# Kernel tuning notes

Measured on AMD Instinct MI355X. Metric: run time of the kernel, lower is better.

Reference implementation:

```python
import jax, jax.numpy as jnp
import numpy as np

F_DIM = 128
EDGE_DIM = 41
N_CONV = 6
N_GRAPHS = 128
EPS = 1e-5


def _bn(h, g, b, m, v):
    # eval-mode BatchNorm1d with running stats
    return (h - m) * (g / jnp.sqrt(v + EPS)) + b


def setup_inputs() -> dict:
    key = jax.random.key(0)
    ks = jax.random.split(key, 40)
    N, E = 20000, 320000
    inp = {}
    inp['x'] = jax.random.normal(ks[0], (N, 98), dtype=jnp.float32)
    inp['edge_index'] = jax.random.randint(ks[1], (2, E), 0, N, dtype=jnp.int32)
    inp['edge_attr'] = jax.random.uniform(ks[2], (E, EDGE_DIM), dtype=jnp.float32)
    inp['batch'] = jnp.sort(jax.random.randint(ks[3], (N,), 0, N_GRAPHS, dtype=jnp.int32))
    s = 0.05
    inp['embed_W'] = jax.random.normal(ks[4], (98, F_DIM), dtype=jnp.float32) * s
    inp['embed_b'] = jnp.zeros((F_DIM,), jnp.float32)
    Z = 2 * F_DIM + EDGE_DIM  # 297
    inp['conv_Wf'] = jax.random.normal(ks[5], (N_CONV, Z, F_DIM), dtype=jnp.float32) * s
    inp['conv_bf'] = jnp.zeros((N_CONV, F_DIM), jnp.float32)
    inp['conv_Ws'] = jax.random.normal(ks[6], (N_CONV, Z, F_DIM), dtype=jnp.float32) * s
    inp['conv_bs'] = jnp.zeros((N_CONV, F_DIM), jnp.float32)
    # inner (CGConv) BN params + running stats
    inp['bn_in_g'] = jnp.ones((N_CONV, F_DIM), jnp.float32)
    inp['bn_in_b'] = jnp.zeros((N_CONV, F_DIM), jnp.float32)
    inp['bn_in_m'] = jax.random.normal(ks[7], (N_CONV, F_DIM), dtype=jnp.float32) * 0.1
    inp['bn_in_v'] = jax.random.uniform(ks[8], (N_CONV, F_DIM), dtype=jnp.float32) + 0.5
    # outer BN params + running stats
    inp['bn_out_g'] = jnp.ones((N_CONV, F_DIM), jnp.float32)
    inp['bn_out_b'] = jnp.zeros((N_CONV, F_DIM), jnp.float32)
    inp['bn_out_m'] = jax.random.normal(ks[9], (N_CONV, F_DIM), dtype=jnp.float32) * 0.1
    inp['bn_out_v'] = jax.random.uniform(ks[10], (N_CONV, F_DIM), dtype=jnp.float32) + 0.5
    inp['pool_W'] = jax.random.normal(ks[11], (2 * F_DIM, F_DIM), dtype=jnp.float32) * s
    inp['pool_b'] = jnp.zeros((F_DIM,), jnp.float32)
    inp['f1_W'] = jax.random.normal(ks[12], (F_DIM, 256), dtype=jnp.float32) * s
    inp['f1_b'] = jnp.zeros((256,), jnp.float32)
    inp['f2_W'] = jax.random.normal(ks[13], (256, 128), dtype=jnp.float32) * s
    inp['f2_b'] = jnp.zeros((128,), jnp.float32)
    inp['f3_W'] = jax.random.normal(ks[14], (128, 1), dtype=jnp.float32) * s
    inp['f3_b'] = jnp.zeros((1,), jnp.float32)
    inp['d1_W'] = jax.random.normal(ks[15], (F_DIM, 256), dtype=jnp.float32) * s
    inp['d1_b'] = jnp.zeros((256,), jnp.float32)
    inp['d2_W'] = jax.random.normal(ks[16], (256, 384), dtype=jnp.float32) * s
    inp['d2_b'] = jnp.zeros((384,), jnp.float32)
    return inp


def reference(x, edge_index, edge_attr, batch,
              embed_W, embed_b,
              conv_Wf, conv_bf, conv_Ws, conv_bs,
              bn_in_g, bn_in_b, bn_in_m, bn_in_v,
              bn_out_g, bn_out_b, bn_out_m, bn_out_v,
              pool_W, pool_b,
              f1_W, f1_b, f2_W, f2_b, f3_W, f3_b,
              d1_W, d1_b, d2_W, d2_b):
    N = x.shape[0]
    src, dst = edge_index[0], edge_index[1]  # PyG: messages flow src(j) -> dst(i)
    h = x @ embed_W + embed_b  # [N, F]
    for i in range(N_CONV):
        h_res = h
        # CGConv: z = [x_i, x_j, e_ij]; m = sigmoid(lin_f(z)) * softplus(lin_s(z))
        z = jnp.concatenate([h[dst], h[src], edge_attr], axis=-1)  # [E, 297]
        m = jax.nn.sigmoid(z @ conv_Wf[i] + conv_bf[i]) * jax.nn.softplus(z @ conv_Ws[i] + conv_bs[i])
        agg = jax.ops.segment_sum(m, dst, num_segments=N)  # scatter-add to target nodes
        agg = _bn(agg, bn_in_g[i], bn_in_b[i], bn_in_m[i], bn_in_v[i])  # CGConv internal BN
        h = agg + h  # CGConv residual
        h = _bn(h, bn_out_g[i], bn_out_b[i], bn_out_m[i], bn_out_v[i])  # outer BN
        if i > 0:
            h = h + h_res
        # dropout: identity in eval mode
    # global mean / max pool by graph id
    sums = jax.ops.segment_sum(h, batch, num_segments=N_GRAPHS)
    counts = jax.ops.segment_sum(jnp.ones((N,), h.dtype), batch, num_segments=N_GRAPHS)
    x_mean = sums / jnp.maximum(counts, 1.0)[:, None]
    x_max = jax.ops.segment_max(h, batch, num_segments=N_GRAPHS)
    x_max = jnp.where(jnp.isfinite(x_max), x_max, 0.0)
    x_pool = jnp.concatenate([x_mean, x_max], axis=-1)  # [B, 2F]
    emb = jax.nn.relu(x_pool @ pool_W + pool_b)  # [B, F]
    f = jax.nn.silu(emb @ f1_W + f1_b)
    f = jax.nn.silu(f @ f2_W + f2_b)
    formation = f @ f3_W + f3_b  # [B, 1]
    d = jax.nn.silu(emb @ d1_W + d1_b)
    dos = (d @ d2_W + d2_b).reshape(-1, 3, 128)  # [B, 3, 128]
    return formation, dos
```

## Files before the change

kernel.cpp:

```cpp
#include <hip/hip_runtime.h>
#include <hip/hip_bf16.h>
#include <math.h>

typedef __attribute__((ext_vector_type(8))) _Float16 half8;
typedef __attribute__((ext_vector_type(4))) _Float16 half4;
typedef __attribute__((ext_vector_type(4))) float f32x4;
typedef __attribute__((ext_vector_type(4))) unsigned int u32x4;

#define FDIM 128
#define EPSBN 1e-5f
#define HSCALE_INV 0.015625f
#define WSCALE 64.0f

__global__ void prep_wn(const float* __restrict__ Wf, const float* __restrict__ Ws,
                        _Float16* __restrict__ Wn) {
    int idx = blockIdx.x * 256 + threadIdx.x;
    const int total = 6 * 4 * 512 * 32;
    if (idx >= total) return;
    int kk = idx & 31;
    int col = (idx >> 5) & 511;
    int c4 = (idx >> 14) & 3;
    int i = idx >> 16;
    int which = col >> 8;
    int colc = col & 255;
    int p = (colc >> 4) & 1;
    int f = ((colc >> 5) << 4) | (colc & 15);
    int ksrc = c4 * 32 + (kk ^ ((colc & 3) << 3));
    int row = which * 128 + ksrc;
    size_t o = ((size_t)i * 297 + row) * 128 + f;
    float v = (p ? Ws[o] : Wf[o]) * WSCALE;
    Wn[idx] = (_Float16)v;
}

__global__ void prep_wb2(const float* __restrict__ Wf, const float* __restrict__ Ws,
                         _Float16* __restrict__ Wb2) {
    int idx = blockIdx.x * 256 + threadIdx.x;
    const int total = 6 * 16384;
    if (idx >= total) return;
    int j = idx & 7;
    int l15 = (idx >> 3) & 15;
    int lhi = (idx >> 7) & 3;
    int cb = (idx >> 9) & 15;
    int c2 = (idx >> 13) & 1;
    int i = idx >> 14;
    int k = c2 * 32 + lhi * 8 + j;
    int colc = cb * 16 + l15;
    int p = (colc >> 4) & 1;
    int f = ((colc >> 5) << 4) | (colc & 15);
    float v = 0.0f;
    if (k < 41) {
        size_t o = ((size_t)i * 297 + 256 + k) * 128 + f;
        v = p ? Ws[o] : Wf[o];
    }
    Wb2[idx] = (_Float16)v;
}

__global__ void prep_bn(const float* __restrict__ bing, const float* __restrict__ binb,
                        const float* __restrict__ binm, const float* __restrict__ binv,
                        const float* __restrict__ bog, const float* __restrict__ bob,
                        const float* __restrict__ bom, const float* __restrict__ bov,
                        float* __restrict__ ABC) {
    int idx = blockIdx.x * 128 + threadIdx.x;
    if (idx >= 6 * 128) return;
    int f = idx & 127;
    int i = idx >> 7;
    int o = i * 128 + f;
    float gin_ = bing[o] / sqrtf(binv[o] + EPSBN);
    float gout_ = bog[o] / sqrtf(bov[o] + EPSBN);
    float A = gin_ * gout_;
    float B = gout_ + ((i > 0) ? 1.0f : 0.0f);
    float C = (binb[o] - binm[o] * gin_ - bom[o]) * gout_ + bob[o];
    ABC[i * 384 + f] = A;
    ABC[i * 384 + 128 + f] = B;
    ABC[i * 384 + 256 + f] = C;
}

__global__ void hist_k(const int* __restrict__ dstI, int* __restrict__ cnt, int E) {
    int e = blockIdx.x * 256 + threadIdx.x;
    if (e < E) atomicAdd(&cnt[dstI[e]], 1);
}

__global__ void scan_k(const int* __restrict__ cnt, int* __restrict__ cursor, int N) {
    __shared__ int part[256];
    int t = threadIdx.x;
    int chunk = (N + 255) / 256;
    int lo = t * chunk, hi = lo + chunk; if (hi > N) hi = N;
    int s = 0;
    for (int i = lo; i < hi; ++i) s += cnt[i];
    part[t] = s;
    __syncthreads();
    for (int d = 1; d < 256; d <<= 1) {
        int v = (t >= d) ? part[t - d] : 0;
        __syncthreads();
        part[t] += v;
        __syncthreads();
    }
    int run = (t > 0) ? part[t - 1] : 0;
    for (int i = lo; i < hi; ++i) { cursor[i] = run; run += cnt[i]; }
}

__global__ void scatter_k(const int* __restrict__ srcI, const int* __restrict__ dstI,
                          int* __restrict__ cursor, unsigned* __restrict__ sdS,
                          int* __restrict__ perm, int E) {
    int e = blockIdx.x * 256 + threadIdx.x;
    if (e >= E) return;
    int d = dstI[e];
    int pos = atomicAdd(&cursor[d], 1);
    sdS[pos] = (unsigned)srcI[e] | ((unsigned)d << 16);
    perm[pos] = e;
}

__global__ void permute_ea(const float* __restrict__ ea, const int* __restrict__ perm,
                           _Float16* __restrict__ eaH, int E) {
    int pos = blockIdx.x * 4 + (threadIdx.x >> 6);
    int c = threadIdx.x & 63;
    if (pos >= E) return;
    int e = perm[pos];
    float v = (c < 41) ? ea[(size_t)e * 41 + c] : 0.0f;
    eaH[(size_t)pos * 64 + c] = (_Float16)v;
}

__global__ void embed_k(const float* __restrict__ x, const float* __restrict__ W,
                        const float* __restrict__ b, float* __restrict__ h, int N) {
    int n = blockIdx.x * 2 + (threadIdx.x >> 7);
    int f = threadIdx.x & 127;
    if (n >= N) return;
    float acc = b[f];
    const float* xr = x + (size_t)n * 98;
    #pragma unroll 7
    for (int k = 0; k < 98; ++k) acc = fmaf(xr[k], W[k * 128 + f], acc);
    h[(size_t)n * 128 + f] = acc;
}

__global__ __launch_bounds__(256, 2)
void node_gemm_f(float* __restrict__ h, float* __restrict__ agg,
                 const _Float16* __restrict__ WnL, const float* __restrict__ ABC,
                 float* __restrict__ Pd4, float* __restrict__ Ps4, int N, int doBN) {
    __shared__ __align__(16) _Float16 ht[32 * 128];
    __shared__ __align__(16) _Float16 wt[512 * 32];
    const int tid = threadIdx.x;
    const int nb = blockIdx.x * 32;

    {
        int e = tid >> 3, t = tid & 7;
        int node = nb + e; bool ok = (node < N); if (!ok) node = N - 1;
        const int c0 = t * 16;
        float* hrow = h + (size_t)node * 128 + c0;
        __align__(16) _Float16 tmp[16];
        if (doBN && ok) {
            float* arow = agg + (size_t)node * 128 + c0;
            #pragma unroll
            for (int u = 0; u < 16; u += 4) {
                f32x4 av = *(const f32x4*)(arow + u);
                f32x4 hv = *(const f32x4*)(hrow + u);
                f32x4 Av = *(const f32x4*)(ABC + c0 + u);
                f32x4 Bv = *(const f32x4*)(ABC + 128 + c0 + u);
                f32x4 Cv = *(const f32x4*)(ABC + 256 + c0 + u);
                f32x4 x;
                #pragma unroll
                for (int j = 0; j < 4; ++j)
                    x[j] = fmaf(av[j], Av[j], fmaf(hv[j], Bv[j], Cv[j]));
                *(f32x4*)(hrow + u) = x;
                *(f32x4*)(arow + u) = (f32x4){0.f, 0.f, 0.f, 0.f};
                #pragma unroll
                for (int j = 0; j < 4; ++j) tmp[u + j] = (_Float16)(x[j] * HSCALE_INV);
            }
        } else {
            #pragma unroll
            for (int u = 0; u < 16; u += 4) {
                f32x4 hv = *(const f32x4*)(hrow + u);
                #pragma unroll
                for (int j = 0; j < 4; ++j) tmp[u + j] = (_Float16)(hv[j] * HSCALE_INV);
            }
        }
        int swz = (e & 7) << 4;
        *(u32x4*)((char*)ht + e * 256 + (((2 * t) * 16) ^ swz)) = *(u32x4*)tmp;
        *(u32x4*)((char*)ht + e * 256 + (((2 * t + 1) * 16) ^ swz)) = *(u32x4*)(tmp + 8);
    }

    f32x4 acc[2][8];
    #pragma unroll
    for (int m = 0; m < 2; ++m)
        #pragma unroll
        for (int n = 0; n < 8; ++n) acc[m][n] = (f32x4){0.f, 0.f, 0.f, 0.f};

    const int wid = tid >> 6;
    const int lane = tid & 63;
    const int l15 = lane & 15;
    const int lhi = lane >> 4;
    const int swzA = (l15 & 7) << 4;

    for (int c4 = 0; c4 < 4; ++c4) {
        const u32x4* gw = (const u32x4*)(WnL + (size_t)c4 * 512 * 32);
        #pragma unroll
        for (int j = 0; j < 8; ++j) ((u32x4*)wt)[tid + 256 * j] = gw[tid + 256 * j];
        __syncthreads();

        half8 a[2];
        #pragma unroll
        for (int m = 0; m < 2; ++m) {
            int r = m * 16 + l15;
            a[m] = *(const half8*)((const char*)ht + r * 256 + ((c4 * 64 + lhi * 16) ^ swzA));
        }
        #pragma unroll
        for (int n = 0; n < 8; ++n) {
            int col = wid * 128 + n * 16 + l15;
            half8 b = *(const half8*)((const char*)wt + col * 64 + ((lhi * 16) ^ ((col & 3) << 4)));
            #pragma unroll
            for (int m = 0; m < 2; ++m)
                acc[m][n] = __builtin_amdgcn_mfma_f32_16x16x32_f16(a[m], b, acc[m][n], 0, 0, 0);
        }
        __syncthreads();
    }

    #pragma unroll
    for (int m = 0; m < 2; ++m) {
        #pragma unroll
        for (int n = 0; n < 8; ++n) {
            int col512 = wid * 128 + n * 16 + l15;
            float* base = (col512 < 256) ? Pd4 : Ps4;
            int c = col512 & 255;
            int g = ((c >> 6) << 4) | (c & 15);
            int q = (c >> 4) & 3;
            #pragma unroll
            for (int j = 0; j < 4; ++j) {
                int node = nb + m * 16 + lhi * 4 + j;
                if (node < N) base[(size_t)node * 256 + g * 4 + q] = acc[m][n][j];
            }
        }
    }
}

__global__ __launch_bounds__(256, 4)
void edge_v7(const _Float16* __restrict__ eaH,
             const unsigned* __restrict__ sdS,
             const _Float16* __restrict__ WbL,
             const float* __restrict__ Pd4, const float* __restrict__ Ps4,
             const float* __restrict__ biasF, const float* __restrict__ biasS,
             float* __restrict__ agg) {
    __shared__ __align__(16) _Float16 eacc[64 * 256];
    __shared__ int srcl[64], dstl[64];

    const int tid = threadIdx.x;
    const int eb = blockIdx.x * 64;

    if (tid < 64) {
        unsigned sd = sdS[eb + tid];
        srcl[tid] = (int)(sd & 0xFFFFu);
        dstl[tid] = (int)(sd >> 16);
    }

    const int wid = tid >> 6;
    const int lane = tid & 63;
    const int l15 = lane & 15;
    const int lhi = lane >> 4;

    f32x4 acc[4][4];
    #pragma unroll
    for (int m = 0; m < 4; ++m)
        #pragma unroll
        for (int n = 0; n < 4; ++n) acc[m][n] = (f32x4){0.f, 0.f, 0.f, 0.f};

    #pragma unroll
    for (int c2 = 0; c2 < 2; ++c2) {
        half8 a[4];
        #pragma unroll
        for (int m = 0; m < 4; ++m) {
            int r = m * 16 + l15;
            a[m] = *(const half8*)(eaH + (size_t)(eb + r) * 64 + c2 * 32 + lhi * 8);
        }
        #pragma unroll
        for (int n = 0; n < 4; ++n) {
            int cb = wid * 4 + n;
            const half8 b = *(const half8*)(WbL +
                            ((((size_t)c2 * 16 + cb) * 4 + lhi) * 16 + l15) * 8);
            #pragma unroll
            for (int m = 0; m < 4; ++m)
                acc[m][n] = __builtin_amdgcn_mfma_f32_16x16x32_f16(a[m], b, acc[m][n], 0, 0, 0);
        }
    }

    {
        const int g = (wid << 4) | l15;
        #pragma unroll
        for (int m = 0; m < 4; ++m) {
            #pragma unroll
            for (int j = 0; j < 4; ++j) {
                int r = m * 16 + lhi * 4 + j;
                half4 hv;
                hv[0] = (_Float16)acc[m][0][j];
                hv[1] = (_Float16)acc[m][1][j];
                hv[2] = (_Float16)acc[m][2][j];
                hv[3] = (_Float16)acc[m][3][j];
                *(half4*)(eacc + r * 256 + g * 4) = hv;
            }
        }
    }
    __syncthreads();

    const int f0 = ((lane >> 4) << 5) | l15;
    const float bF0 = biasF[f0], bF1 = biasF[f0 + 16];
    const float bS0 = biasS[f0], bS1 = biasS[f0 + 16];
    const int rbase = wid * 16;

    float s0 = 0.f, s1 = 0.f;
    int prevd = dstl[rbase];
    f32x4 pdv = *(const f32x4*)(Pd4 + (size_t)prevd * 256 + lane * 4);
    f32x4 psv_n = *(const f32x4*)(Ps4 + (size_t)srcl[rbase] * 256 + lane * 4);

    #pragma unroll
    for (int e = 0; e < 16; ++e) {
        int r = rbase + e;
        int d = dstl[r];
        if (d != prevd) {
            pdv = *(const f32x4*)(Pd4 + (size_t)d * 256 + lane * 4);
            prevd = d;
        }
        f32x4 psv = psv_n;
        if (e < 15)
            psv_n = *(const f32x4*)(Ps4 + (size_t)srcl[r + 1] * 256 + lane * 4);
        half4 ev = *(const half4*)(eacc + r * 256 + lane * 4);
        float fp0 = (float)ev[0] + pdv[0] + psv[0] + bF0;
        float sp0 = (float)ev[1] + pdv[1] + psv[1] + bS0;
        float fp1 = (float)ev[2] + pdv[2] + psv[2] + bF1;
        float sp1 = (float)ev[3] + pdv[3] + psv[3] + bS1;
        float m0 = __builtin_amdgcn_rcpf(1.0f + __expf(-fp0)) *
                   (fmaxf(sp0, 0.0f) + __logf(1.0f + __expf(-fabsf(sp0))));
        float m1 = __builtin_amdgcn_rcpf(1.0f + __expf(-fp1)) *
                   (fmaxf(sp1, 0.0f) + __logf(1.0f + __expf(-fabsf(sp1))));
        s0 += m0;
        s1 += m1;
        bool flush = (e == 15) || (dstl[r + 1] != d);
        if (flush) {
            atomicAdd(&agg[(size_t)d * 128 + f0], s0);
            atomicAdd(&agg[(size_t)d * 128 + f0 + 16], s1);
            s0 = 0.f; s1 = 0.f;
        }
    }
}

__global__ void bn_final(const float* __restrict__ agg, float* __restrict__ h,
                         const float* __restrict__ ABC, int n128) {
    int idx = blockIdx.x * 256 + threadIdx.x;
    if (idx >= n128) return;
    int f = idx & 127;
    h[idx] = fmaf(agg[idx], ABC[f], fmaf(h[idx], ABC[128 + f], ABC[256 + f]));
}

__global__ __launch_bounds__(256, 4)
void pool2_k(const float* __restrict__ h, const int* __restrict__ batch,
             float* __restrict__ sums, unsigned* __restrict__ maxs,
             float* __restrict__ counts, int N) {
    const int f = threadIdx.x & 127;
    const int half = threadIdx.x >> 7;
    const int nb = blockIdx.x * 64 + half * 32;
    if (nb >= N) return;

    float s = 0.f;
    float mx = -3.4e38f;
    int prevg = -1;
    int runlen = 0;

    for (int e = 0; e < 32; ++e) {
        int n = nb + e;
        if (n >= N) break;
        int g = batch[n];
        if (g != prevg) {
            if (prevg >= 0) {
                atomicAdd(&sums[prevg * 128 + f], s);
                unsigned u = __float_as_uint(mx);
                unsigned key = (u & 0x80000000u) ? ~u : (u | 0x80000000u);
                atomicMax(&maxs[prevg * 128 + f], key);
                if (f == 0) atomicAdd(&counts[prevg], (float)runlen);
            }
            s = 0.f; mx = -3.4e38f; runlen = 0; prevg = g;
        }
        float v = h[(size_t)n * 128 + f];
        s += v;
        mx = fmaxf(mx, v);
        ++runlen;
    }
    if (prevg >= 0) {
        atomicAdd(&sums[prevg * 128 + f], s);
        unsigned u = __float_as_uint(mx);
        unsigned key = (u & 0x80000000u) ? ~u : (u | 0x80000000u);
        atomicMax(&maxs[prevg * 128 + f], key);
        if (f == 0) atomicAdd(&counts[prevg], (float)runlen);
    }
}

__global__ __launch_bounds__(256)
void head_k(const float* __restrict__ sums, const unsigned* __restrict__ maxs,
            const float* __restrict__ counts,
            const float* __restrict__ pW, const float* __restrict__ pb,
            const float* __restrict__ f1W, const float* __restrict__ f1b,
            const float* __restrict__ f2W, const float* __restrict__ f2b,
            const float* __restrict__ f3W, const float* __restrict__ f3b,
            const float* __restrict__ d1W, const float* __restrict__ d1b,
            const float* __restrict__ d2W, const float* __restrict__ d2b,
            float* __restrict__ out) {
    __shared__ float xp[256], emb[128], s1[256], s2[128], dd[256];
    int g = blockIdx.x, t = threadIdx.x;
    float cnt = counts[g];
    if (t < 128) {
        float mean = sums[g * 128 + t] / fmaxf(cnt, 1.0f);
        float mx = 0.0f;
        if (cnt > 0.0f) {
            unsigned key = maxs[g * 128 + t];
            unsigned u = (key & 0x80000000u) ? (key & 0x7fffffffu) : ~key;
            mx = __uint_as_float(u);
            if (!isfinite(mx)) mx = 0.0f;
        }
        xp[t] = mean;
        xp[128 + t] = mx;
    }
    __syncthreads();
    if (t < 128) {
        float a = pb[t];
        for (int k = 0; k < 256; ++k) a = fmaf(xp[k], pW[k * 128 + t], a);
        emb[t] = fmaxf(a, 0.0f);
    }
    __syncthreads();
    {
        float a = f1b[t];
        for (int k = 0; k < 128; ++k) a = fmaf(emb[k], f1W[k * 256 + t], a);
        s1[t] = a / (1.0f + __expf(-a));
    }
    __syncthreads();
    if (t < 128) {
        float a = f2b[t];
        for (int k = 0; k < 256; ++k) a = fmaf(s1[k], f2W[k * 128 + t], a);
        s2[t] = a / (1.0f + __expf(-a));
    }
    {
        float a = d1b[t];
        for (int k = 0; k < 128; ++k) a = fmaf(emb[k], d1W[k * 256 + t], a);
        dd[t] = a / (1.0f + __expf(-a));
    }
    __syncthreads();
    if (t == 0) {
        float a = f3b[0];
        for (int k = 0; k < 128; ++k) a = fmaf(s2[k], f3W[k], a);
        out[g] = a;
    }
    for (int o = t; o < 384; o += 256) {
        float a = d2b[o];
        for (int k = 0; k < 256; ++k) a = fmaf(dd[k], d2W[k * 384 + o], a);
        out[128 + (size_t)g * 384 + o] = a;
    }
}

extern "C" void kernel_launch(void* const* d_in, const int* in_sizes, int n_in,
                              void* d_out, int out_size, void* d_ws, size_t ws_size,
                              hipStream_t stream) {
    const float* x       = (const float*)d_in[0];
    const int*   eidx    = (const int*)d_in[1];
    const float* ea      = (const float*)d_in[2];
    const int*   batch   = (const int*)d_in[3];
    const float* embW    = (const float*)d_in[4];
    const float* embB    = (const float*)d_in[5];
    const float* convWf  = (const float*)d_in[6];
    const float* convbf  = (const float*)d_in[7];
    const float* convWs  = (const float*)d_in[8];
    const float* convbs  = (const float*)d_in[9];
    const float* bing    = (const float*)d_in[10];
    const float* binb    = (const float*)d_in[11];
    const float* binm    = (const float*)d_in[12];
    const float* binv    = (const float*)d_in[13];
    const float* bog     = (const float*)d_in[14];
    const float* bob     = (const float*)d_in[15];
    const float* bom     = (const float*)d_in[16];
    const float* bov     = (const float*)d_in[17];
    const float* pW      = (const float*)d_in[18];
    const float* pb      = (const float*)d_in[19];
    const float* f1W     = (const float*)d_in[20];
    const float* f1b     = (const float*)d_in[21];
    const float* f2W     = (const float*)d_in[22];
    const float* f2b     = (const float*)d_in[23];
    const float* f3W     = (const float*)d_in[24];
    const float* f3b     = (const float*)d_in[25];
    const float* d1W     = (const float*)d_in[26];
    const float* d1b     = (const float*)d_in[27];
    const float* d2W     = (const float*)d_in[28];
    const float* d2b     = (const float*)d_in[29];

    const int N = in_sizes[0] / 98;
    const int E = in_sizes[1] / 2;
    const int* srcI = eidx;
    const int* dstI = eidx + E;

    char* ws = (char*)d_ws;
    float* h        = (float*)(ws);
    float* agg      = (float*)(ws + 10240000);
    float* Pd4      = (float*)(ws + 20480000);
    float* Ps4      = (float*)(ws + 40960000);
    _Float16* Wn    = (_Float16*)(ws + 61440000);
    _Float16* Wb2   = (_Float16*)(ws + 62226432);
    float* sums     = (float*)(ws + 62423040);
    unsigned* maxs  = (unsigned*)(ws + 62488576);
    float* gcnt     = (float*)(ws + 62554112);
    unsigned* sdS   = (unsigned*)(ws + 62554624);
    int* perm       = (int*)(ws + 63834624);
    _Float16* eaH   = (_Float16*)(ws + 65114624);
    float* ABC      = (float*)(ws + 106074624);
    int* nodeCnt    = (int*)(ws + 20480000);
    int* cursor     = nodeCnt + N;

    prep_wn<<<(6 * 4 * 512 * 32) / 256, 256, 0, stream>>>(convWf, convWs, Wn);
    prep_wb2<<<(6 * 16384 + 255) / 256, 256, 0, stream>>>(convWf, convWs, Wb2);
    prep_bn<<<6, 128, 0, stream>>>(bing, binb, binm, binv, bog, bob, bom, bov, ABC);
    hipMemsetAsync(nodeCnt, 0, (size_t)N * 4, stream);
    hist_k<<<(E + 255) / 256, 256, 0, stream>>>(dstI, nodeCnt, E);
    scan_k<<<1, 256, 0, stream>>>(nodeCnt, cursor, N);
    scatter_k<<<(E + 255) / 256, 256, 0, stream>>>(srcI, dstI, cursor, sdS, perm, E);
    permute_ea<<<(E + 3) / 4, 256, 0, stream>>>(ea, perm, eaH, E);
    embed_k<<<(N + 1) / 2, 256, 0, stream>>>(x, embW, embB, h, N);

    const int n128 = N * 128;
    const int nblk = (N + 31) / 32;
    hipMemsetAsync(agg, 0, (size_t)n128 * 4, stream);
    for (int i = 0; i < 6; ++i) {
        node_gemm_f<<<nblk, 256, 0, stream>>>(h, agg, Wn + (size_t)i * 4 * 512 * 32,
                                              ABC + (size_t)(i - 1) * 384,
                                              Pd4, Ps4, N, (i > 0) ? 1 : 0);
        edge_v7<<<E / 64, 256, 0, stream>>>(eaH, sdS,
                                            Wb2 + (size_t)i * 16384,
                                            Pd4, Ps4, convbf + i * 128, convbs + i * 128, agg);
    }
    bn_final<<<(n128 + 255) / 256, 256, 0, stream>>>(agg, h, ABC + 5 * 384, n128);

    hipMemsetAsync(sums, 0, 65536 + 65536 + 512, stream);
    pool2_k<<<(N + 63) / 64, 256, 0, stream>>>(h, batch, sums, maxs, gcnt, N);
    head_k<<<128, 256, 0, stream>>>(sums, maxs, gcnt, pW, pb,
                                    f1W, f1b, f2W, f2b, f3W, f3b,
                                    d1W, d1b, d2W, d2b, (float*)d_out);
}
```

Measured before the change: 789.8 us.

## Use MFMA for embedding and load node-GEMM weights directly in fragment layout

```diff
diff --git a/kernel.cpp b/kernel.cpp
--- a/kernel.cpp
+++ b/kernel.cpp
@@ -12,24 +12,26 @@
 #define HSCALE_INV 0.015625f
 #define WSCALE 64.0f
 
-__global__ void prep_wn(const float* __restrict__ Wf, const float* __restrict__ Ws,
-                        _Float16* __restrict__ Wn) {
+__global__ void prep_wn2(const float* __restrict__ Wf, const float* __restrict__ Ws,
+                         _Float16* __restrict__ Wn2) {
     int idx = blockIdx.x * 256 + threadIdx.x;
-    const int total = 6 * 4 * 512 * 32;
+    const int total = 6 * 65536;
     if (idx >= total) return;
-    int kk = idx & 31;
-    int col = (idx >> 5) & 511;
+    int j = idx & 7;
+    int l15 = (idx >> 3) & 15;
+    int lhi = (idx >> 7) & 3;
+    int cb = (idx >> 9) & 31;
     int c4 = (idx >> 14) & 3;
     int i = idx >> 16;
-    int which = col >> 8;
-    int colc = col & 255;
+    int col512 = cb * 16 + l15;
+    int which = col512 >> 8;
+    int colc = col512 & 255;
     int p = (colc >> 4) & 1;
     int f = ((colc >> 5) << 4) | (colc & 15);
-    int ksrc = c4 * 32 + (kk ^ ((colc & 3) << 3));
-    int row = which * 128 + ksrc;
+    int k = c4 * 32 + lhi * 8 + j;
+    int row = which * 128 + k;
     size_t o = ((size_t)i * 297 + row) * 128 + f;
-    float v = (p ? Ws[o] : Wf[o]) * WSCALE;
-    Wn[idx] = (_Float16)v;
+    Wn2[idx] = (_Float16)((p ? Ws[o] : Wf[o]) * WSCALE);
 }
 
 __global__ void prep_wb2(const float* __restrict__ Wf, const float* __restrict__ Ws,
@@ -55,6 +57,19 @@
     Wb2[idx] = (_Float16)v;
 }
 
+__global__ void prep_we(const float* __restrict__ embW, _Float16* __restrict__ We) {
+    int idx = blockIdx.x * 256 + threadIdx.x;
+    if (idx >= 16384) return;
+    int j = idx & 7;
+    int l15 = (idx >> 3) & 15;
+    int lhi = (idx >> 7) & 3;
+    int cb = (idx >> 9) & 7;
+    int c4 = (idx >> 12) & 3;
+    int k = c4 * 32 + lhi * 8 + j;
+    int f = cb * 16 + l15;
+    We[idx] = (_Float16)((k < 98) ? embW[k * 128 + f] : 0.0f);
+}
+
 __global__ void prep_bn(const float* __restrict__ bing, const float* __restrict__ binb,
                         const float* __restrict__ binm, const float* __restrict__ binv,
                         const float* __restrict__ bog, const float* __restrict__ bob,
@@ -67,12 +82,9 @@
     int o = i * 128 + f;
     float gin_ = bing[o] / sqrtf(binv[o] + EPSBN);
     float gout_ = bog[o] / sqrtf(bov[o] + EPSBN);
-    float A = gin_ * gout_;
-    float B = gout_ + ((i > 0) ? 1.0f : 0.0f);
-    float C = (binb[o] - binm[o] * gin_ - bom[o]) * gout_ + bob[o];
-    ABC[i * 384 + f] = A;
-    ABC[i * 384 + 128 + f] = B;
-    ABC[i * 384 + 256 + f] = C;
+    ABC[i * 384 + f] = gin_ * gout_;
+    ABC[i * 384 + 128 + f] = gout_ + ((i > 0) ? 1.0f : 0.0f);
+    ABC[i * 384 + 256 + f] = (binb[o] - binm[o] * gin_ - bom[o]) * gout_ + bob[o];
 }
 
 __global__ void hist_k(const int* __restrict__ dstI, int* __restrict__ cnt, int E) {
@@ -120,24 +132,79 @@
     eaH[(size_t)pos * 64 + c] = (_Float16)v;
 }
 
-__global__ void embed_k(const float* __restrict__ x, const float* __restrict__ W,
-                        const float* __restrict__ b, float* __restrict__ h, int N) {
-    int n = blockIdx.x * 2 + (threadIdx.x >> 7);
-    int f = threadIdx.x & 127;
-    if (n >= N) return;
-    float acc = b[f];
-    const float* xr = x + (size_t)n * 98;
-    #pragma unroll 7
-    for (int k = 0; k < 98; ++k) acc = fmaf(xr[k], W[k * 128 + f], acc);
-    h[(size_t)n * 128 + f] = acc;
-}
-
-__global__ __launch_bounds__(256, 2)
+__global__ __launch_bounds__(256, 4)
+void embed_mm(const float* __restrict__ x, const _Float16* __restrict__ We,
+              const float* __restrict__ b, float* __restrict__ h, int N) {
+    __shared__ __align__(16) _Float16 xt[32 * 128];
+    const int tid = threadIdx.x;
+    const int nb = blockIdx.x * 32;
+
+    {
+        int e = tid >> 3, t = tid & 7;
+        int node = nb + e; if (node >= N) node = N - 1;
+        const float* row = x + (size_t)node * 98;
+        __align__(16) _Float16 tmp[16];
+        #pragma unroll
+        for (int u = 0; u < 16; ++u) {
+            int c = t * 16 + u;
+            tmp[u] = (c < 98) ? (_Float16)row[c] : (_Float16)0.f;
+        }
+        int swz = (e & 7) << 4;
+        *(u32x4*)((char*)xt + e * 256 + (((2 * t) * 16) ^ swz)) = *(u32x4*)tmp;
+        *(u32x4*)((char*)xt + e * 256 + (((2 * t + 1) * 16) ^ swz)) = *(u32x4*)(tmp + 8);
+    }
+    __syncthreads();
+
+    const int wid = tid >> 6;
+    const int lane = tid & 63;
+    const int l15 = lane & 15;
+    const int lhi = lane >> 4;
+    const int swzA = (l15 & 7) << 4;
+
+    f32x4 acc[2][2];
+    #pragma unroll
+    for (int m = 0; m < 2; ++m)
+        #pragma unroll
+        for (int n = 0; n < 2; ++n) acc[m][n] = (f32x4){0.f, 0.f, 0.f, 0.f};
+
+    #pragma unroll
+    for (int c4 = 0; c4 < 4; ++c4) {
+        half8 a[2];
+        #pragma unroll
+        for (int m = 0; m < 2; ++m) {
+            int r = m * 16 + l15;
+            a[m] = *(const half8*)((const char*)xt + r * 256 + ((c4 * 64 + lhi * 16) ^ swzA));
+        }
+        #pragma unroll
+        for (int n = 0; n < 2; ++n) {
+            int cb = wid * 2 + n;
+            const half8 bf = *(const half8*)(We + ((((size_t)c4 * 8 + cb) * 4 + lhi) * 16 + l15) * 8);
+            #pragma unroll
+            for (int m = 0; m < 2; ++m)
+                acc[m][n] = __builtin_amdgcn_mfma_f32_16x16x32_f16(a[m], bf, acc[m][n], 0, 0, 0);
+        }
+    }
+
+    #pragma unroll
+    for (int m = 0; m < 2; ++m) {
+        #pragma unroll
+        for (int n = 0; n < 2; ++n) {
+            int feat = wid * 32 + n * 16 + l15;
+            float bias = b[feat];
+            #pragma unroll
+            for (int j = 0; j < 4; ++j) {
+                int node = nb + m * 16 + lhi * 4 + j;
+                if (node < N) h[(size_t)node * 128 + feat] = acc[m][n][j] + bias;
+            }
+        }
+    }
+}
+
+__global__ __launch_bounds__(256, 4)
 void node_gemm_f(float* __restrict__ h, float* __restrict__ agg,
                  const _Float16* __restrict__ WnL, const float* __restrict__ ABC,
                  float* __restrict__ Pd4, float* __restrict__ Ps4, int N, int doBN) {
     __shared__ __align__(16) _Float16 ht[32 * 128];
-    __shared__ __align__(16) _Float16 wt[512 * 32];
     const int tid = threadIdx.x;
     const int nb = blockIdx.x * 32;
 
@@ -156,14 +223,14 @@
                 f32x4 Av = *(const f32x4*)(ABC + c0 + u);
                 f32x4 Bv = *(const f32x4*)(ABC + 128 + c0 + u);
                 f32x4 Cv = *(const f32x4*)(ABC + 256 + c0 + u);
-                f32x4 x;
+                f32x4 xv;
                 #pragma unroll
                 for (int j = 0; j < 4; ++j)
-                    x[j] = fmaf(av[j], Av[j], fmaf(hv[j], Bv[j], Cv[j]));
-                *(f32x4*)(hrow + u) = x;
+                    xv[j] = fmaf(av[j], Av[j], fmaf(hv[j], Bv[j], Cv[j]));
+                *(f32x4*)(hrow + u) = xv;
                 *(f32x4*)(arow + u) = (f32x4){0.f, 0.f, 0.f, 0.f};
                 #pragma unroll
-                for (int j = 0; j < 4; ++j) tmp[u + j] = (_Float16)(x[j] * HSCALE_INV);
+                for (int j = 0; j < 4; ++j) tmp[u + j] = (_Float16)(xv[j] * HSCALE_INV);
             }
         } else {
             #pragma unroll
@@ -177,6 +244,7 @@
         *(u32x4*)((char*)ht + e * 256 + (((2 * t) * 16) ^ swz)) = *(u32x4*)tmp;
         *(u32x4*)((char*)ht + e * 256 + (((2 * t + 1) * 16) ^ swz)) = *(u32x4*)(tmp + 8);
     }
+    __syncthreads();
 
     f32x4 acc[2][8];
     #pragma unroll
@@ -190,12 +258,8 @@
     const int lhi = lane >> 4;
     const int swzA = (l15 & 7) << 4;
 
+    #pragma unroll
     for (int c4 = 0; c4 < 4; ++c4) {
-        const u32x4* gw = (const u32x4*)(WnL + (size_t)c4 * 512 * 32);
-        #pragma unroll
-        for (int j = 0; j < 8; ++j) ((u32x4*)wt)[tid + 256 * j] = gw[tid + 256 * j];
-        __syncthreads();
-
         half8 a[2];
         #pragma unroll
         for (int m = 0; m < 2; ++m) {
@@ -204,13 +268,13 @@
         }
         #pragma unroll
         for (int n = 0; n < 8; ++n) {
-            int col = wid * 128 + n * 16 + l15;
-            half8 b = *(const half8*)((const char*)wt + col * 64 + ((lhi * 16) ^ ((col & 3) << 4)));
+            int cb = wid * 8 + n;
+            const half8 bf = *(const half8*)(WnL +
+                             ((((size_t)c4 * 32 + cb) * 4 + lhi) * 16 + l15) * 8);
             #pragma unroll
             for (int m = 0; m < 2; ++m)
-                acc[m][n] = __builtin_amdgcn_mfma_f32_16x16x32_f16(a[m], b, acc[m][n], 0, 0, 0);
-        }
-        __syncthreads();
+                acc[m][n] = __builtin_amdgcn_mfma_f32_16x16x32_f16(a[m], bf, acc[m][n], 0, 0, 0);
+        }
     }
 
     #pragma unroll
@@ -494,7 +558,7 @@
     float* agg      = (float*)(ws + 10240000);
     float* Pd4      = (float*)(ws + 20480000);
     float* Ps4      = (float*)(ws + 40960000);
-    _Float16* Wn    = (_Float16*)(ws + 61440000);
+    _Float16* Wn2   = (_Float16*)(ws + 61440000);
     _Float16* Wb2   = (_Float16*)(ws + 62226432);
     float* sums     = (float*)(ws + 62423040);
     unsigned* maxs  = (unsigned*)(ws + 62488576);
@@ -503,24 +567,27 @@
     int* perm       = (int*)(ws + 63834624);
     _Float16* eaH   = (_Float16*)(ws + 65114624);
     float* ABC      = (float*)(ws + 106074624);
+    _Float16* We    = (_Float16*)(ws + 106083840);
     int* nodeCnt    = (int*)(ws + 20480000);
     int* cursor     = nodeCnt + N;
 
-    prep_wn<<<(6 * 4 * 512 * 32) / 256, 256, 0, stream>>>(convWf, convWs, Wn);
+    prep_wn2<<<(6 * 65536) / 256, 256, 0, stream>>>(convWf, convWs, Wn2);
     prep_wb2<<<(6 * 16384 + 255) / 256, 256, 0, stream>>>(convWf, convWs, Wb2);
+    prep_we<<<64, 256, 0, stream>>>(embW, We);
     prep_bn<<<6, 128, 0, stream>>>(bing, binb, binm, binv, bog, bob, bom, bov, ABC);
     hipMemsetAsync(nodeCnt, 0, (size_t)N * 4, stream);
     hist_k<<<(E + 255) / 256, 256, 0, stream>>>(dstI, nodeCnt, E);
     scan_k<<<1, 256, 0, stream>>>(nodeCnt, cursor, N);
     scatter_k<<<(E + 255) / 256, 256, 0, stream>>>(srcI, dstI, cursor, sdS, perm, E);
     permute_ea<<<(E + 3) / 4, 256, 0, stream>>>(ea, perm, eaH, E);
-    embed_k<<<(N + 1) / 2, 256, 0, stream>>>(x, embW, embB, h, N);
 
     const int n128 = N * 128;
     const int nblk = (N + 31) / 32;
+    embed_mm<<<nblk, 256, 0, stream>>>(x, We, embB, h, N);
+
     hipMemsetAsync(agg, 0, (size_t)n128 * 4, stream);
     for (int i = 0; i < 6; ++i) {
-        node_gemm_f<<<nblk, 256, 0, stream>>>(h, agg, Wn + (size_t)i * 4 * 512 * 32,
+        node_gemm_f<<<nblk, 256, 0, stream>>>(h, agg, Wn2 + (size_t)i * 65536,
                                               ABC + (size_t)(i - 1) * 384,
                                               Pd4, Ps4, N, (i > 0) ? 1 : 0);
         edge_v7<<<E / 64, 256, 0, stream>>>(eaH, sdS,
```

Result: faster. 739.1 us (-6.4%).
